# Kernel optimization log

Measured on AMD Instinct MI355X. Metric: run time of the kernel, lower is better.

## Reference

```python
import jax, jax.numpy as jnp
import numpy as np

DIM = 1024
NUM_HEADS = 16
HEAD_DIM = DIM // NUM_HEADS


def setup_inputs() -> dict:
    key = jax.random.key(0)
    ks = jax.random.split(key, 5)
    x = jax.random.normal(ks[0], (2, 4096, DIM), dtype=jnp.float32)
    # nn.Linear(dim, 3*dim): weight [3D, D], bias [3D]; we store transposed [D, 3D]
    scale = 1.0 / np.sqrt(DIM)
    w_qkv = jax.random.normal(ks[1], (DIM, 3 * DIM), dtype=jnp.float32) * scale
    b_qkv = jax.random.normal(ks[2], (3 * DIM,), dtype=jnp.float32) * scale
    w_o = jax.random.normal(ks[3], (DIM, DIM), dtype=jnp.float32) * scale
    b_o = jax.random.normal(ks[4], (DIM,), dtype=jnp.float32) * scale
    return {"x": x, "w_qkv": w_qkv, "b_qkv": b_qkv, "w_o": w_o, "b_o": b_o}


def reference(x, w_qkv, b_qkv, w_o, b_o):
    b, n, _ = x.shape
    h, d = NUM_HEADS, HEAD_DIM
    qkv = x @ w_qkv + b_qkv                      # [B, N, 3D]
    q, k, v = jnp.split(qkv, 3, axis=-1)
    # [B, N, H, d] -> [B, H, N, d]
    q = q.reshape(b, n, h, d).transpose(0, 2, 1, 3)
    k = k.reshape(b, n, h, d).transpose(0, 2, 1, 3)
    v = v.reshape(b, n, h, d).transpose(0, 2, 1, 3)
    scale = 1.0 / np.sqrt(d).astype(np.float32)
    score = jnp.einsum("bhqd,bhkd->bhqk", q, k) * scale   # [B, H, N, N]
    attn = jax.nn.softmax(score, axis=-1)
    out = jnp.einsum("bhqk,bhkd->bhqd", attn, v)          # [B, H, N, d]
    out = out.transpose(0, 2, 1, 3).reshape(b, n, h * d)  # [B, N, D]
    return out @ w_o + b_o
```

## Files before the change

kernel.cpp:

```cpp
#include <hip/hip_runtime.h>

typedef __attribute__((ext_vector_type(8))) __bf16 bf16x8;
typedef __attribute__((ext_vector_type(8))) short short8;
typedef __attribute__((ext_vector_type(4))) float f32x4;

__device__ __forceinline__ unsigned short f2bf(float f) {
    union { float f; unsigned int i; } c; c.f = f;
    unsigned int r = c.i + 0x7fffu + ((c.i >> 16) & 1u);
    return (unsigned short)(r >> 16);
}

#if __has_builtin(__builtin_amdgcn_exp2f)
#define FAST_EXP2(x) __builtin_amdgcn_exp2f(x)
#else
#define FAST_EXP2(x) __expf((x) * 0.6931471805599453f)
#endif

__device__ __forceinline__ void async_cp16(const unsigned short* g, unsigned short* l) {
    __builtin_amdgcn_global_load_lds(
        (const __attribute__((address_space(1))) unsigned int*)g,
        (__attribute__((address_space(3))) unsigned int*)l, 16, 0, 0);
}

#define DIM 1024
#define NSEQ 4096
#define NH 16
#define HD 64
#define KPAD 72

__global__ __launch_bounds__(256)
void conv_kernel(const float* __restrict__ in, unsigned short* __restrict__ out)
{
    const int i = blockIdx.x * 256 + threadIdx.x;
    const float4 a0 = ((const float4*)in)[i * 2];
    const float4 a1 = ((const float4*)in)[i * 2 + 1];
    short8 v;
    v[0] = (short)f2bf(a0.x); v[1] = (short)f2bf(a0.y);
    v[2] = (short)f2bf(a0.z); v[3] = (short)f2bf(a0.w);
    v[4] = (short)f2bf(a1.x); v[5] = (short)f2bf(a1.y);
    v[6] = (short)f2bf(a1.z); v[7] = (short)f2bf(a1.w);
    ((short8*)out)[i] = v;
}

template<int N, int K>
__global__ __launch_bounds__(256)
void transpose_conv_kernel(const float* __restrict__ in, unsigned short* __restrict__ out)
{
    __shared__ unsigned short Ls[64][65];
    const int t  = threadIdx.x;
    const int k0 = blockIdx.x * 64, n0 = blockIdx.y * 64;
    const int kl = t >> 2, nl = (t & 3) * 16;
    const float* src = in + (size_t)(k0 + kl) * N + n0 + nl;
    #pragma unroll
    for (int i = 0; i < 4; i++) {
        float4 a = *(const float4*)(src + i * 4);
        Ls[kl][nl + i*4 + 0] = f2bf(a.x); Ls[kl][nl + i*4 + 1] = f2bf(a.y);
        Ls[kl][nl + i*4 + 2] = f2bf(a.z); Ls[kl][nl + i*4 + 3] = f2bf(a.w);
    }
    __syncthreads();
    const int kl2 = (t & 7) * 8;
    #pragma unroll
    for (int i = 0; i < 2; i++) {
        const int nl2 = (t >> 3) + i * 32;
        short8 v;
        #pragma unroll
        for (int j = 0; j < 8; j++) v[j] = (short)Ls[kl2 + j][nl2];
        *(short8*)(out + (size_t)(n0 + nl2) * K + k0 + kl2) = v;
    }
}

template<int MODE>
__global__ __launch_bounds__(256)
void gemm_kernel(const unsigned short* __restrict__ A,
                 const unsigned short* __restrict__ Bt,
                 const float* __restrict__ bias,
                 unsigned short* __restrict__ out0,
                 unsigned short* __restrict__ out1,
                 unsigned short* __restrict__ out2,
                 float* __restrict__ outf)
{
    __shared__ __align__(16) unsigned short As[128][32];
    __shared__ __align__(16) unsigned short Bs[128][32];
    const int t    = threadIdx.x;
    const int m0   = blockIdx.x * 128, n0 = blockIdx.y * 128;
    const int lane = t & 63, wv = t >> 6;
    const int l15  = lane & 15, quad = lane >> 4;
    const int wm   = (wv >> 1) * 64, wn = (wv & 1) * 64;
    const int sr   = wv * 16 + (lane >> 2);
    const int sc   = (lane & 3) * 8;
    const unsigned short* Ag = A  + (size_t)m0 * 1024;
    const unsigned short* Bg = Bt + (size_t)n0 * 1024;

    f32x4 acc[4][4] = {};

    for (int kt = 0; kt < 1024; kt += 32) {
        __syncthreads();
        async_cp16(Ag + (size_t)(sr)      * 1024 + kt + sc, &As[sr][sc]);
        async_cp16(Ag + (size_t)(sr + 64) * 1024 + kt + sc, &As[sr + 64][sc]);
        async_cp16(Bg + (size_t)(sr)      * 1024 + kt + sc, &Bs[sr][sc]);
        async_cp16(Bg + (size_t)(sr + 64) * 1024 + kt + sc, &Bs[sr + 64][sc]);
        __syncthreads();

        bf16x8 af[4], bfr[4];
        #pragma unroll
        for (int mi = 0; mi < 4; mi++) af[mi]  = *(const bf16x8*)&As[wm + mi*16 + l15][quad*8];
        #pragma unroll
        for (int ni = 0; ni < 4; ni++) bfr[ni] = *(const bf16x8*)&Bs[wn + ni*16 + l15][quad*8];
        #pragma unroll
        for (int mi = 0; mi < 4; mi++)
            #pragma unroll
            for (int ni = 0; ni < 4; ni++)
                acc[mi][ni] = __builtin_amdgcn_mfma_f32_16x16x32_bf16(af[mi], bfr[ni], acc[mi][ni], 0, 0, 0);
    }

    #pragma unroll
    for (int mi = 0; mi < 4; mi++) {
        #pragma unroll
        for (int ni = 0; ni < 4; ni++) {
            const int col  = n0 + wn + ni*16 + l15;
            const float bval = bias[col];
            #pragma unroll
            for (int r = 0; r < 4; r++) {
                const int row = m0 + wm + mi*16 + quad*4 + r;
                const float val = acc[mi][ni][r] + bval;
                if (MODE == 0) {
                    const int which = col >> 10;
                    const int rem   = col & 1023;
                    const int h = rem >> 6, dd = rem & 63;
                    const int bb = row >> 12, ns = row & 4095;
                    if (which == 2) {
                        out2[((size_t)((bb * NH + h) * HD + dd)) * NSEQ + ns] = f2bf(val);
                    } else {
                        const size_t off = ((size_t)((bb * NH + h) * NSEQ + ns)) * HD + dd;
                        ((which == 0) ? out0 : out1)[off] = f2bf(val);
                    }
                } else {
                    outf[(size_t)row * 1024 + col] = val;
                }
            }
        }
    }
}

#define C_LOG2E 0.1803368801111183f
#define M_LOG2  11.541560327111707f

__global__ __launch_bounds__(256, 4)
void attn_kernel(const unsigned short* __restrict__ qb,
                 const unsigned short* __restrict__ kb,
                 const unsigned short* __restrict__ vb,
                 unsigned short* __restrict__ ob)
{
    __shared__ __align__(16) unsigned short Ks[64][KPAD];
    __shared__ __align__(16) unsigned short Vt[64][KPAD];
    __shared__ __align__(16) unsigned short Ps[4][32][KPAD];

    const int t    = threadIdx.x;
    const int wv   = t >> 6, lane = t & 63, l15 = lane & 15, quad = lane >> 4;
    const int q0   = blockIdx.x * 128;
    const int h    = blockIdx.y, b = blockIdx.z;
    const size_t bh = (size_t)(b * NH + h) * NSEQ * HD;
    const unsigned short* Qp  = qb + bh;
    const unsigned short* Kp  = kb + bh;
    const unsigned short* Vtp = vb + bh;

    bf16x8 aq[2][2];
    #pragma unroll
    for (int mi = 0; mi < 2; mi++) {
        const unsigned short* qrow =
            Qp + (size_t)(q0 + wv*32 + mi*16 + l15) * HD + quad*8;
        aq[mi][0] = *(const bf16x8*)(qrow);
        aq[mi][1] = *(const bf16x8*)(qrow + 32);
    }

    float l_loc[2][4] = {};
    f32x4 acc_o[2][4] = {};

    const int sr = t >> 2, sc = (t & 3) * 16;

    for (int kt = 0; kt < NSEQ; kt += 64) {
        short8 kv0 = *(const short8*)(Kp  + (size_t)(kt + sr) * HD + sc);
        short8 kv1 = *(const short8*)(Kp  + (size_t)(kt + sr) * HD + sc + 8);
        short8 vv0 = *(const short8*)(Vtp + (size_t)sr * NSEQ + kt + sc);
        short8 vv1 = *(const short8*)(Vtp + (size_t)sr * NSEQ + kt + sc + 8);
        __syncthreads();
        *(short8*)&Ks[sr][sc]     = kv0;
        *(short8*)&Ks[sr][sc + 8] = kv1;
        *(short8*)&Vt[sr][sc]     = vv0;
        *(short8*)&Vt[sr][sc + 8] = vv1;
        __syncthreads();

        f32x4 accs[2][4] = {};
        #pragma unroll
        for (int nj = 0; nj < 4; nj++) {
            bf16x8 bk0 = *(const bf16x8*)&Ks[nj*16 + l15][quad*8];
            bf16x8 bk1 = *(const bf16x8*)&Ks[nj*16 + l15][32 + quad*8];
            #pragma unroll
            for (int mi = 0; mi < 2; mi++) {
                accs[mi][nj] = __builtin_amdgcn_mfma_f32_16x16x32_bf16(aq[mi][0], bk0, accs[mi][nj], 0, 0, 0);
                accs[mi][nj] = __builtin_amdgcn_mfma_f32_16x16x32_bf16(aq[mi][1], bk1, accs[mi][nj], 0, 0, 0);
            }
        }

        #pragma unroll
        for (int mi = 0; mi < 2; mi++) {
            #pragma unroll
            for (int r = 0; r < 4; r++) {
                const int prow = mi*16 + quad*4 + r;
                float lsum = 0.f;
                #pragma unroll
                for (int nj = 0; nj < 4; nj++) {
                    const float p = FAST_EXP2(fmaf(accs[mi][nj][r], C_LOG2E, -M_LOG2));
                    const unsigned int pb = __float_as_uint(p);
                    Ps[wv][prow][nj*16 + l15] = (unsigned short)(pb >> 16);
                    lsum += __uint_as_float(pb & 0xffff0000u);
                }
                l_loc[mi][r] += lsum;
            }
        }

        bf16x8 ap[2][2];
        #pragma unroll
        for (int mi = 0; mi < 2; mi++) {
            ap[mi][0] = *(const bf16x8*)&Ps[wv][mi*16 + l15][quad*8];
            ap[mi][1] = *(const bf16x8*)&Ps[wv][mi*16 + l15][32 + quad*8];
        }
        #pragma unroll
        for (int nj = 0; nj < 4; nj++) {
            bf16x8 bv0 = *(const bf16x8*)&Vt[nj*16 + l15][quad*8];
            bf16x8 bv1 = *(const bf16x8*)&Vt[nj*16 + l15][32 + quad*8];
            #pragma unroll
            for (int mi = 0; mi < 2; mi++) {
                acc_o[mi][nj] = __builtin_amdgcn_mfma_f32_16x16x32_bf16(ap[mi][0], bv0, acc_o[mi][nj], 0, 0, 0);
                acc_o[mi][nj] = __builtin_amdgcn_mfma_f32_16x16x32_bf16(ap[mi][1], bv1, acc_o[mi][nj], 0, 0, 0);
            }
        }
    }

    #pragma unroll
    for (int mi = 0; mi < 2; mi++) {
        #pragma unroll
        for (int r = 0; r < 4; r++) {
            float l = l_loc[mi][r];
            #pragma unroll
            for (int off = 1; off < 16; off <<= 1) l += __shfl_xor(l, off);
            const float inv = 1.0f / l;
            const int row = q0 + wv*32 + mi*16 + quad*4 + r;
            const size_t base = ((size_t)(b * NSEQ + row)) * DIM + h * HD;
            #pragma unroll
            for (int nj = 0; nj < 4; nj++)
                ob[base + nj*16 + l15] = f2bf(acc_o[mi][nj][r] * inv);
        }
    }
}

extern "C" void kernel_launch(void* const* d_in, const int* in_sizes, int n_in,
                              void* d_out, int out_size, void* d_ws, size_t ws_size,
                              hipStream_t stream)
{
    const float *x = nullptr, *w_qkv = nullptr, *b_qkv = nullptr,
                *w_o = nullptr, *b_o = nullptr;
    for (int i = 0; i < n_in; i++) {
        switch (in_sizes[i]) {
            case 8388608: x     = (const float*)d_in[i]; break;
            case 3145728: w_qkv = (const float*)d_in[i]; break;
            case 3072:    b_qkv = (const float*)d_in[i]; break;
            case 1048576: w_o   = (const float*)d_in[i]; break;
            case 1024:    b_o   = (const float*)d_in[i]; break;
        }
    }
    float* out = (float*)d_out;

    const size_t WQB  = (size_t)3072 * 1024;
    const size_t WOB  = (size_t)1024 * 1024;
    const size_t SEGB = (size_t)NSEQ * DIM;

    char* p = (char*)d_ws;
    unsigned short* wqb = (unsigned short*)p;  p += WQB * 2;
    unsigned short* wob = (unsigned short*)p;  p += WOB * 2;

    transpose_conv_kernel<3072, 1024><<<dim3(16, 48), 256, 0, stream>>>(w_qkv, wqb);
    transpose_conv_kernel<1024, 1024><<<dim3(16, 16), 256, 0, stream>>>(w_o, wob);

    const size_t tier1_bytes = (WQB + WOB + 2*SEGB + 3*2*SEGB) * 2;
    if (ws_size >= tier1_bytes) {
        unsigned short* xb = (unsigned short*)p;  p += 2 * SEGB * 2;
        unsigned short* qb = (unsigned short*)p;  p += 2 * SEGB * 2;
        unsigned short* kb = (unsigned short*)p;  p += 2 * SEGB * 2;
        unsigned short* vb = (unsigned short*)p;
        unsigned short* ao = xb;
        conv_kernel<<<4096, 256, 0, stream>>>(x, xb);
        gemm_kernel<0><<<dim3(64, 24), 256, 0, stream>>>(xb, wqb, b_qkv, qb, kb, vb, nullptr);
        attn_kernel<<<dim3(32, NH, 2), 256, 0, stream>>>(qb, kb, vb, ao);
        gemm_kernel<1><<<dim3(64, 8), 256, 0, stream>>>(ao, wob, b_o, nullptr, nullptr, nullptr, out);
    } else {
        unsigned short* xb = (unsigned short*)p;  p += SEGB * 2;
        unsigned short* qb = (unsigned short*)p;  p += SEGB * 2;
        unsigned short* kb = (unsigned short*)p;  p += SEGB * 2;
        unsigned short* vb = (unsigned short*)p;
        unsigned short* ao = xb;
        for (int b = 0; b < 2; b++) {
            conv_kernel<<<2048, 256, 0, stream>>>(x + b * SEGB, xb);
            gemm_kernel<0><<<dim3(32, 24), 256, 0, stream>>>(xb, wqb, b_qkv, qb, kb, vb, nullptr);
            attn_kernel<<<dim3(32, NH, 1), 256, 0, stream>>>(qb, kb, vb, ao);
            gemm_kernel<1><<<dim3(32, 8), 256, 0, stream>>>(ao, wob, b_o, nullptr, nullptr, nullptr, out + b * SEGB);
        }
    }
}
```

Baseline: 390.0 us.

## Prefetch next K/V tile into registers, transpose S MFMA, pack P writes

Moves the global loads of the next K/V tile to right after the LDS store barrier, so they overlap with the current tile's compute. Swaps the MFMA operands so each lane holds four consecutive key columns of one query row. That lets P be written as packed bf16 pairs with v_cvt_pk_bf16 in a single 8-byte store, and cuts row-sum shuffles to two xors plus a broadcast. Also adds s_setprio around the MFMA blocks and an explicit lgkmcnt wait. The cost is more live registers. The row sums also change slightly, because they now add unrounded fp32 p instead of the truncated bf16 values used in the PV product, and P is rounded rather than truncated.

```diff
diff --git a/kernel.cpp b/kernel.cpp
--- a/kernel.cpp
+++ b/kernel.cpp
@@ -8,6 +8,12 @@
     union { float f; unsigned int i; } c; c.f = f;
     unsigned int r = c.i + 0x7fffu + ((c.i >> 16) & 1u);
     return (unsigned short)(r >> 16);
+}
+
+__device__ __forceinline__ unsigned int cvt_pk_bf16(float lo, float hi) {
+    unsigned int r;
+    asm("v_cvt_pk_bf16_f32 %0, %1, %2" : "=v"(r) : "v"(lo), "v"(hi));
+    return r;
 }
 
 #if __has_builtin(__builtin_amdgcn_exp2f)
@@ -173,16 +179,17 @@
         aq[mi][1] = *(const bf16x8*)(qrow + 32);
     }
 
-    float l_loc[2][4] = {};
+    float l_loc[2] = {};
     f32x4 acc_o[2][4] = {};
 
     const int sr = t >> 2, sc = (t & 3) * 16;
 
+    short8 kv0 = *(const short8*)(Kp  + (size_t)sr * HD + sc);
+    short8 kv1 = *(const short8*)(Kp  + (size_t)sr * HD + sc + 8);
+    short8 vv0 = *(const short8*)(Vtp + (size_t)sr * NSEQ + sc);
+    short8 vv1 = *(const short8*)(Vtp + (size_t)sr * NSEQ + sc + 8);
+
     for (int kt = 0; kt < NSEQ; kt += 64) {
-        short8 kv0 = *(const short8*)(Kp  + (size_t)(kt + sr) * HD + sc);
-        short8 kv1 = *(const short8*)(Kp  + (size_t)(kt + sr) * HD + sc + 8);
-        short8 vv0 = *(const short8*)(Vtp + (size_t)sr * NSEQ + kt + sc);
-        short8 vv1 = *(const short8*)(Vtp + (size_t)sr * NSEQ + kt + sc + 8);
         __syncthreads();
         *(short8*)&Ks[sr][sc]     = kv0;
         *(short8*)&Ks[sr][sc + 8] = kv1;
@@ -190,34 +197,43 @@
         *(short8*)&Vt[sr][sc + 8] = vv1;
         __syncthreads();
 
+        const int ktn = (kt + 64) & (NSEQ - 1);
+        kv0 = *(const short8*)(Kp  + (size_t)(ktn + sr) * HD + sc);
+        kv1 = *(const short8*)(Kp  + (size_t)(ktn + sr) * HD + sc + 8);
+        vv0 = *(const short8*)(Vtp + (size_t)sr * NSEQ + ktn + sc);
+        vv1 = *(const short8*)(Vtp + (size_t)sr * NSEQ + ktn + sc + 8);
+
         f32x4 accs[2][4] = {};
+        __builtin_amdgcn_s_setprio(1);
         #pragma unroll
         for (int nj = 0; nj < 4; nj++) {
             bf16x8 bk0 = *(const bf16x8*)&Ks[nj*16 + l15][quad*8];
             bf16x8 bk1 = *(const bf16x8*)&Ks[nj*16 + l15][32 + quad*8];
             #pragma unroll
             for (int mi = 0; mi < 2; mi++) {
-                accs[mi][nj] = __builtin_amdgcn_mfma_f32_16x16x32_bf16(aq[mi][0], bk0, accs[mi][nj], 0, 0, 0);
-                accs[mi][nj] = __builtin_amdgcn_mfma_f32_16x16x32_bf16(aq[mi][1], bk1, accs[mi][nj], 0, 0, 0);
+                accs[mi][nj] = __builtin_amdgcn_mfma_f32_16x16x32_bf16(bk0, aq[mi][0], accs[mi][nj], 0, 0, 0);
+                accs[mi][nj] = __builtin_amdgcn_mfma_f32_16x16x32_bf16(bk1, aq[mi][1], accs[mi][nj], 0, 0, 0);
             }
         }
+        __builtin_amdgcn_s_setprio(0);
 
         #pragma unroll
         for (int mi = 0; mi < 2; mi++) {
             #pragma unroll
-            for (int r = 0; r < 4; r++) {
-                const int prow = mi*16 + quad*4 + r;
-                float lsum = 0.f;
-                #pragma unroll
-                for (int nj = 0; nj < 4; nj++) {
-                    const float p = FAST_EXP2(fmaf(accs[mi][nj][r], C_LOG2E, -M_LOG2));
-                    const unsigned int pb = __float_as_uint(p);
-                    Ps[wv][prow][nj*16 + l15] = (unsigned short)(pb >> 16);
-                    lsum += __uint_as_float(pb & 0xffff0000u);
-                }
-                l_loc[mi][r] += lsum;
+            for (int nj = 0; nj < 4; nj++) {
+                const float p0 = FAST_EXP2(fmaf(accs[mi][nj][0], C_LOG2E, -M_LOG2));
+                const float p1 = FAST_EXP2(fmaf(accs[mi][nj][1], C_LOG2E, -M_LOG2));
+                const float p2 = FAST_EXP2(fmaf(accs[mi][nj][2], C_LOG2E, -M_LOG2));
+                const float p3 = FAST_EXP2(fmaf(accs[mi][nj][3], C_LOG2E, -M_LOG2));
+                l_loc[mi] += (p0 + p1) + (p2 + p3);
+                uint2 w;
+                w.x = cvt_pk_bf16(p0, p1);
+                w.y = cvt_pk_bf16(p2, p3);
+                *(uint2*)&Ps[wv][mi*16 + l15][nj*16 + quad*4] = w;
             }
         }
+        asm volatile("s_waitcnt lgkmcnt(0)" ::: "memory");
+        __builtin_amdgcn_sched_barrier(0);
 
         bf16x8 ap[2][2];
         #pragma unroll
@@ -225,6 +241,7 @@
             ap[mi][0] = *(const bf16x8*)&Ps[wv][mi*16 + l15][quad*8];
             ap[mi][1] = *(const bf16x8*)&Ps[wv][mi*16 + l15][32 + quad*8];
         }
+        __builtin_amdgcn_s_setprio(1);
         #pragma unroll
         for (int nj = 0; nj < 4; nj++) {
             bf16x8 bv0 = *(const bf16x8*)&Vt[nj*16 + l15][quad*8];
@@ -235,16 +252,17 @@
                 acc_o[mi][nj] = __builtin_amdgcn_mfma_f32_16x16x32_bf16(ap[mi][1], bv1, acc_o[mi][nj], 0, 0, 0);
             }
         }
+        __builtin_amdgcn_s_setprio(0);
     }
 
     #pragma unroll
     for (int mi = 0; mi < 2; mi++) {
+        float l = l_loc[mi];
+        l += __shfl_xor(l, 16);
+        l += __shfl_xor(l, 32);
         #pragma unroll
         for (int r = 0; r < 4; r++) {
-            float l = l_loc[mi][r];
-            #pragma unroll
-            for (int off = 1; off < 16; off <<= 1) l += __shfl_xor(l, off);
-            const float inv = 1.0f / l;
+            const float inv = 1.0f / __shfl(l, quad*4 + r, 16);
             const int row = q0 + wv*32 + mi*16 + quad*4 + r;
             const size_t base = ((size_t)(b * NSEQ + row)) * DIM + h * HD;
             #pragma unroll
```

Result: no change. 390.1 us (+0.0%).
